# Kernel optimization log

Hardware: AMD Instinct MI355X
Metric: run time of the kernel (lower is better)

## Reference

```python
import jax, jax.numpy as jnp
import numpy as np

N_NODES = 100000
N_EDGES = 1600000
N_GRAPHS = 5000
NODE_DIM = 16
EDGE_DIM = 16
HID = 20


def setup_inputs() -> dict:
    key = jax.random.key(0)
    ks = jax.random.split(key, 12)
    edge_index = jax.random.randint(ks[0], (2, N_EDGES), 0, N_NODES)
    node_attr = jax.random.normal(ks[1], (N_NODES, NODE_DIM), dtype=jnp.float32)
    edge_attr = jax.random.normal(ks[2], (N_EDGES, EDGE_DIM), dtype=jnp.float32)
    batch = jnp.sort(jax.random.randint(ks[3], (N_NODES,), 0, N_GRAPHS))
    s = 0.1
    W_msg = jax.random.normal(ks[4], (2 * NODE_DIM + EDGE_DIM, HID), dtype=jnp.float32) * s
    b_msg = jnp.zeros((HID,), dtype=jnp.float32)
    W1 = jax.random.normal(ks[5], (HID, 10), dtype=jnp.float32) * s
    b1 = jnp.zeros((10,), dtype=jnp.float32)
    W2 = jax.random.normal(ks[6], (10, 10), dtype=jnp.float32) * s
    b2 = jnp.zeros((10,), dtype=jnp.float32)
    W3 = jax.random.normal(ks[7], (10, 1), dtype=jnp.float32) * s
    b3 = jnp.zeros((1,), dtype=jnp.float32)
    return {"edge_index": edge_index, "node_attr": node_attr, "edge_attr": edge_attr,
            "batch": batch, "W_msg": W_msg, "b_msg": b_msg, "W1": W1, "b1": b1,
            "W2": W2, "b2": b2, "W3": W3, "b3": b3}


def reference(edge_index, node_attr, edge_attr, batch,
              W_msg, b_msg, W1, b1, W2, b2, W3, b3):
    src, dst = edge_index[0], edge_index[1]
    # MPL_1: gather -> linear -> relu -> scatter-sum to destination nodes
    feats = jnp.concatenate([node_attr[src], node_attr[dst], edge_attr], axis=-1)  # [E, 48]
    msg = jax.nn.relu(feats @ W_msg + b_msg)  # [E, 20]
    x = jax.ops.segment_sum(msg, dst, num_segments=N_NODES)  # [N, 20]
    # node MLP + graph pooling (segment_coo sum over batch) + graph MLP
    x = jax.nn.relu(x @ W1 + b1)  # [N, 10]
    g = jax.ops.segment_sum(x, batch, num_segments=N_GRAPHS)  # [G, 10]
    g = jax.nn.relu(g @ W2 + b2)
    return g @ W3 + b3  # [G, 1]
```

## Files before the change

kernel.cpp:

```cpp
#include <hip/hip_runtime.h>

constexpr int NN = 100000;
constexpr int NE = 1600000;
constexpr int NG = 5000;
constexpr int BKT = 64;
constexpr int NBKT = (NN + BKT - 1) / BKT;
constexpr int NB = 128;
constexpr int CHUNK = NE / NB;

typedef float v2f __attribute__((ext_vector_type(2)));

constexpr size_t OFF_G  = 0;
constexpr size_t OFF_BH = 50048;
constexpr size_t OFF_ST = OFF_BH + (size_t)NB * NBKT;
constexpr size_t OFF_PM = OFF_ST + NBKT + 1;
constexpr size_t OFF_SP = OFF_PM + NE;
constexpr size_t OFF_EP = ((OFF_SP + NE) + 15) & ~(size_t)15;
constexpr size_t NEED_WORDS = OFF_EP + (size_t)NE * 16;

__global__ __launch_bounds__(256) void k_hist(const int* __restrict__ ei,
                                              int* __restrict__ bh,
                                              float* __restrict__ g) {
  __shared__ int lh[NBKT];
  for (int i = threadIdx.x; i < NBKT; i += 256) lh[i] = 0;
  __syncthreads();
  const int* dstp = ei + NE;
  int s = blockIdx.x * CHUNK;
  for (int i = s + threadIdx.x; i < s + CHUNK; i += 256)
    atomicAdd(&lh[dstp[i] >> 6], 1);
  int gid = blockIdx.x * 256 + threadIdx.x;
  if (gid < 12500) ((float4*)g)[gid] = make_float4(0.f, 0.f, 0.f, 0.f);
  __syncthreads();
  int* out = bh + (size_t)blockIdx.x * NBKT;
  for (int k = threadIdx.x; k < NBKT; k += 256) out[k] = lh[k];
}

__global__ __launch_bounds__(256) void k_btot(const int* __restrict__ bh,
                                              int* __restrict__ starts) {
  int k = blockIdx.x * 256 + threadIdx.x;
  if (k >= NBKT) return;
  int tot = 0;
  for (int b = 0; b < NB; b += 4) {
    int a0 = bh[(size_t)(b    ) * NBKT + k];
    int a1 = bh[(size_t)(b + 1) * NBKT + k];
    int a2 = bh[(size_t)(b + 2) * NBKT + k];
    int a3 = bh[(size_t)(b + 3) * NBKT + k];
    tot += a0 + a1 + a2 + a3;
  }
  starts[k] = tot;
}

__global__ __launch_bounds__(1024) void k_sscan(int* __restrict__ starts) {
  __shared__ int s0[1024], s1[1024];
  int t = threadIdx.x;
  int k0 = 2 * t, k1 = 2 * t + 1;
  int tot0 = (k0 < NBKT) ? starts[k0] : 0;
  int tot1 = (k1 < NBKT) ? starts[k1] : 0;
  int ssum = tot0 + tot1;
  int* cur = s0; int* nxt = s1;
  cur[t] = ssum;
  __syncthreads();
  for (int off = 1; off < 1024; off <<= 1) {
    int v = cur[t];
    if (t >= off) v += cur[t - off];
    nxt[t] = v;
    __syncthreads();
    int* tmp = cur; cur = nxt; nxt = tmp;
  }
  int excl = cur[t] - ssum;
  if (k0 < NBKT) starts[k0] = excl;
  if (k1 <= NBKT) starts[k1] = excl + tot0;
}

__global__ __launch_bounds__(256) void k_bases(int* __restrict__ bh,
                                               const int* __restrict__ starts) {
  int k = blockIdx.x * 256 + threadIdx.x;
  if (k >= NBKT) return;
  int run = starts[k];
  for (int b = 0; b < NB; ++b) {
    size_t idx = (size_t)b * NBKT + k;
    int v = bh[idx];
    bh[idx] = run;
    run += v;
  }
}

template <bool PRE>
__global__ __launch_bounds__(256) void k_scatter(const int* __restrict__ ei,
                                                 const int* __restrict__ bh,
                                                 int* __restrict__ pm) {
  __shared__ int base[NBKT];
  __shared__ int cnt[NBKT];
  const int* row = bh + (size_t)blockIdx.x * NBKT;
  for (int k = threadIdx.x; k < NBKT; k += 256) { base[k] = row[k]; cnt[k] = 0; }
  __syncthreads();
  const int* dstp = ei + NE;
  int s = blockIdx.x * CHUNK;
  for (int i = s + threadIdx.x; i < s + CHUNK; i += 256) {
    int d = dstp[i];
    int k = d >> 6;
    int r = atomicAdd(&cnt[k], 1);
    int slot = base[k] + r;
    if (PRE) pm[i] = slot | ((d & 63) << 25);
    else     pm[slot] = i | ((d & 63) << 24);
  }
}

__global__ __launch_bounds__(256) void k_reorder(const int* __restrict__ ei,
                                                 const float* __restrict__ eattr,
                                                 const int* __restrict__ inv,
                                                 float* __restrict__ ep_,
                                                 int* __restrict__ srcp) {
  int gid = blockIdx.x * 256 + threadIdx.x;
  int e = gid >> 2, part = gid & 3;
  if (e >= NE) return;
  int iv = inv[e];
  int slot = iv & 0x1FFFFFF;
  float4 v = ((const float4*)eattr)[(size_t)e * 4 + part];
  ((float4*)ep_)[(size_t)slot * 4 + part] = v;
  if (part == 0) srcp[slot] = ei[e] | ((iv >> 25) << 24);
}

#define PK4(V, K0) \
  a0 = __builtin_elementwise_fma(v2f{(V).x, (V).x}, W[K0+0], a0); \
  a1 = __builtin_elementwise_fma(v2f{(V).y, (V).y}, W[K0+1], a1); \
  a2 = __builtin_elementwise_fma(v2f{(V).z, (V).z}, W[K0+2], a2); \
  a3 = __builtin_elementwise_fma(v2f{(V).w, (V).w}, W[K0+3], a3);

template <bool PRE>
__global__ __launch_bounds__(256, 3) void k_edge(
    const int* __restrict__ ei,
    const float* __restrict__ nattr,
    const float* __restrict__ eattr,
    const float* __restrict__ Wm,
    const float* __restrict__ bm,
    const int* __restrict__ batch,
    const float* __restrict__ W1,
    const float* __restrict__ b1,
    const int* __restrict__ pm,
    const int* __restrict__ starts,
    float* __restrict__ g) {
  __shared__ float xt[20 * 65];
  __shared__ float gb[64 * 10];
  __shared__ float4 wt4[250];
  __shared__ float4 us4[64 * 5];
  __shared__ int s_se[2];
  __shared__ int s_bmin;
  int tid = threadIdx.x;
  for (int i = tid; i < 20 * 65; i += 256) xt[i] = 0.f;
  for (int i = tid; i < 640; i += 256) gb[i] = 0.f;
  if (tid < 240) {
    int j = tid / 24, t = tid - j * 24, k = 2 * t;
    wt4[j * 25 + t] = make_float4(Wm[k * 20 + 2 * j],       Wm[k * 20 + 2 * j + 1],
                                  Wm[(k + 1) * 20 + 2 * j], Wm[(k + 1) * 20 + 2 * j + 1]);
  }
  int nbase = blockIdx.x * BKT;
  {
    int dl = tid >> 2, part = tid & 3;
    int row = min(nbase + dl, NN - 1);
    us4[dl * 5 + part] = ((const float4*)nattr)[(size_t)row * 4 + part];
  }
  if (tid < 2) s_se[tid] = starts[blockIdx.x + tid];
  if (tid == 0) s_bmin = batch[nbase];
  __syncthreads();
  int is = s_se[0], ie = s_se[1];

  int wave = tid >> 6;
  int lane = tid & 63;
  int ep = lane / 10;
  int jp = lane - ep * 10;
  bool act = ep < 6;
  int epc = act ? ep : 0;

  v2f bj = {bm[2 * jp], bm[2 * jp + 1]};

  v2f W[48];
#pragma unroll
  for (int t = 0; t < 24; ++t) {
    float4 q = wt4[jp * 25 + t];
    W[2 * t]     = v2f{q.x, q.y};
    W[2 * t + 1] = v2f{q.z, q.w};
  }
#pragma unroll
  for (int k = 0; k < 48; ++k) asm volatile("" : "+v"(W[k]));

  int base = is + wave * 6;
  int sp0 = 0, sp1 = 0, sp2 = 0, sv0 = 0;
  if (base < ie) {
    sp0 = pm[min(base + epc, ie - 1)];
    sp1 = (base + 24 < ie) ? pm[min(base + 24 + epc, ie - 1)] : sp0;
    sp2 = (base + 48 < ie) ? pm[min(base + 48 + epc, ie - 1)] : sp1;
    if (!PRE) sv0 = ei[sp0 & 0xFFFFFF];
  }
  while (base < ie) {
    int sp3 = (base + 72 < ie) ? pm[min(base + 72 + epc, ie - 1)] : sp2;
    int svN = 0;
    if (!PRE) svN = (base + 24 < ie) ? ei[sp1 & 0xFFFFFF] : sv0;

    size_t eidx = PRE ? (size_t)min(base + epc, ie - 1)
                      : (size_t)(sp0 & 0xFFFFFF);
    int src = PRE ? (sp0 & 0xFFFFFF) : sv0;
    const float4* pe = (const float4*)eattr + eidx * 4;
    const float4* ps = (const float4*)nattr + (size_t)src * 4;
    float4 e0 = pe[0], e1 = pe[1], e2 = pe[2], e3 = pe[3];
    float4 n0 = ps[0], n1 = ps[1], n2 = ps[2], n3 = ps[3];
    int dl = (sp0 >> 24) & 63;
    float4 u0 = us4[dl * 5 + 0], u1 = us4[dl * 5 + 1];
    float4 u2 = us4[dl * 5 + 2], u3 = us4[dl * 5 + 3];

    v2f a0 = {0.f, 0.f}, a1 = {0.f, 0.f}, a2 = {0.f, 0.f}, a3 = {0.f, 0.f};
    PK4(n0, 0)  PK4(n1, 4)  PK4(n2, 8)  PK4(n3, 12)
    PK4(u0, 16) PK4(u1, 20) PK4(u2, 24) PK4(u3, 28)
    PK4(e0, 32) PK4(e1, 36) PK4(e2, 40) PK4(e3, 44)
    v2f r = ((a0 + a1) + (a2 + a3)) + bj;

    bool valid = act && (base + epc < ie);
    float m0 = fmaxf(r.x, 0.f);
    float m1 = fmaxf(r.y, 0.f);
    if (valid && m0 > 0.f) atomicAdd(&xt[(2 * jp) * 65 + dl], m0);
    if (valid && m1 > 0.f) atomicAdd(&xt[(2 * jp + 1) * 65 + dl], m1);

    base += 24; sp0 = sp1; sp1 = sp2; sp2 = sp3; sv0 = svN;
  }
  __syncthreads();

  int nn = min(BKT, NN - nbase);
  int bmin = s_bmin;
  if (tid < 64 && tid < nn) {
    int node = tid;
    float xi[20];
#pragma unroll
    for (int j = 0; j < 20; ++j) xi[j] = xt[j * 65 + node];
    float acc[10];
#pragma unroll
    for (int j = 0; j < 10; ++j) acc[j] = b1[j];
#pragma unroll
    for (int k = 0; k < 20; ++k) {
      float fk = xi[k];
#pragma unroll
      for (int j = 0; j < 10; ++j) acc[j] = fmaf(fk, W1[k * 10 + j], acc[j]);
    }
    int bn = batch[nbase + node];
    int d = bn - bmin;
    if (d < 64) {
#pragma unroll
      for (int j = 0; j < 10; ++j) {
        float m = fmaxf(acc[j], 0.f);
        if (m > 0.f) atomicAdd(&gb[d * 10 + j], m);
      }
    } else {
#pragma unroll
      for (int j = 0; j < 10; ++j) {
        float m = fmaxf(acc[j], 0.f);
        if (m > 0.f) unsafeAtomicAdd(&g[(size_t)bn * 10 + j], m);
      }
    }
  }
  __syncthreads();
  int glim = min(640, NG * 10 - bmin * 10);
  float* gp = g + (size_t)bmin * 10;
  for (int idx = tid; idx < glim; idx += 256) {
    float v = gb[idx];
    if (v != 0.f) unsafeAtomicAdd(&gp[idx], v);
  }
}

__global__ __launch_bounds__(256) void k_graph(
    const float* __restrict__ g,
    const float* __restrict__ W2, const float* __restrict__ b2,
    const float* __restrict__ W3, const float* __restrict__ b3,
    float* __restrict__ out) {
  int i = blockIdx.x * 256 + threadIdx.x;
  if (i >= NG) return;
  float gi[10];
  const float2* pg = (const float2*)(g + (size_t)i * 10);
#pragma unroll
  for (int k = 0; k < 5; ++k) { float2 v = pg[k]; gi[2*k] = v.x; gi[2*k+1] = v.y; }
  float o = b3[0];
#pragma unroll
  for (int j = 0; j < 10; ++j) {
    float a = b2[j];
#pragma unroll
    for (int k = 0; k < 10; ++k) a = fmaf(gi[k], W2[k * 10 + j], a);
    o = fmaf(fmaxf(a, 0.f), W3[j], o);
  }
  out[i] = o;
}

extern "C" void kernel_launch(void* const* d_in, const int* in_sizes, int n_in,
                              void* d_out, int out_size, void* d_ws, size_t ws_size,
                              hipStream_t stream) {
  const int*   ei    = (const int*)  d_in[0];
  const float* nattr = (const float*)d_in[1];
  const float* eattr = (const float*)d_in[2];
  const int*   batch = (const int*)  d_in[3];
  const float* Wm    = (const float*)d_in[4];
  const float* bm    = (const float*)d_in[5];
  const float* W1    = (const float*)d_in[6];
  const float* b1    = (const float*)d_in[7];
  const float* W2    = (const float*)d_in[8];
  const float* b2    = (const float*)d_in[9];
  const float* W3    = (const float*)d_in[10];
  const float* b3    = (const float*)d_in[11];

  float* g      = (float*)d_ws + OFF_G;
  int*   bh     = (int*)d_ws + OFF_BH;
  int*   starts = (int*)d_ws + OFF_ST;
  int*   pm     = (int*)d_ws + OFF_PM;
  int*   srcp   = (int*)d_ws + OFF_SP;
  float* ep_    = (float*)d_ws + OFF_EP;

  bool pre = ws_size >= NEED_WORDS * 4;

  constexpr int SCAN_BLKS = (NBKT + 255) / 256;

  k_hist   <<<NB, 256, 0, stream>>>(ei, bh, g);
  k_btot   <<<SCAN_BLKS, 256, 0, stream>>>(bh, starts);
  k_sscan  <<<1, 1024, 0, stream>>>(starts);
  k_bases  <<<SCAN_BLKS, 256, 0, stream>>>(bh, starts);
  if (pre) {
    k_scatter<true><<<NB, 256, 0, stream>>>(ei, bh, pm);
    k_reorder<<<(NE * 4 + 255) / 256, 256, 0, stream>>>(ei, eattr, pm, ep_, srcp);
    k_edge<true><<<NBKT, 256, 0, stream>>>(ei, nattr, ep_, Wm, bm, batch, W1, b1,
                                           srcp, starts, g);
  } else {
    k_scatter<false><<<NB, 256, 0, stream>>>(ei, bh, pm);
    k_edge<false><<<NBKT, 256, 0, stream>>>(ei, nattr, eattr, Wm, bm, batch, W1, b1,
                                            pm, starts, g);
  }
  k_graph  <<<(NG + 255) / 256, 256, 0, stream>>>(g, W2, b2, W3, b3, (float*)d_out);
}
```

Baseline: 382.7 us.

## Fuse edge reorder into scatter and software-pipeline edge/node loads in k_edge

```diff
diff --git a/kernel.cpp b/kernel.cpp
--- a/kernel.cpp
+++ b/kernel.cpp
@@ -88,7 +88,10 @@
 template <bool PRE>
 __global__ __launch_bounds__(256) void k_scatter(const int* __restrict__ ei,
                                                  const int* __restrict__ bh,
-                                                 int* __restrict__ pm) {
+                                                 int* __restrict__ pm,
+                                                 const float* __restrict__ eattr,
+                                                 float* __restrict__ ep_,
+                                                 int* __restrict__ srcp) {
   __shared__ int base[NBKT];
   __shared__ int cnt[NBKT];
   const int* row = bh + (size_t)blockIdx.x * NBKT;
@@ -101,24 +104,16 @@
     int k = d >> 6;
     int r = atomicAdd(&cnt[k], 1);
     int slot = base[k] + r;
-    if (PRE) pm[i] = slot | ((d & 63) << 25);
-    else     pm[slot] = i | ((d & 63) << 24);
-  }
-}
-
-__global__ __launch_bounds__(256) void k_reorder(const int* __restrict__ ei,
-                                                 const float* __restrict__ eattr,
-                                                 const int* __restrict__ inv,
-                                                 float* __restrict__ ep_,
-                                                 int* __restrict__ srcp) {
-  int gid = blockIdx.x * 256 + threadIdx.x;
-  int e = gid >> 2, part = gid & 3;
-  if (e >= NE) return;
-  int iv = inv[e];
-  int slot = iv & 0x1FFFFFF;
-  float4 v = ((const float4*)eattr)[(size_t)e * 4 + part];
-  ((float4*)ep_)[(size_t)slot * 4 + part] = v;
-  if (part == 0) srcp[slot] = ei[e] | ((iv >> 25) << 24);
+    if (PRE) {
+      srcp[slot] = ei[i] | ((d & 63) << 24);
+      const float4* src4 = (const float4*)eattr + (size_t)i * 4;
+      float4 v0 = src4[0], v1 = src4[1], v2 = src4[2], v3 = src4[3];
+      float4* dst4 = (float4*)ep_ + (size_t)slot * 4;
+      dst4[0] = v0; dst4[1] = v1; dst4[2] = v2; dst4[3] = v3;
+    } else {
+      pm[slot] = i | ((d & 63) << 24);
+    }
+  }
 }
 
 #define PK4(V, K0) \
@@ -128,7 +123,7 @@
   a3 = __builtin_elementwise_fma(v2f{(V).w, (V).w}, W[K0+3], a3);
 
 template <bool PRE>
-__global__ __launch_bounds__(256, 3) void k_edge(
+__global__ __launch_bounds__(256, 2) void k_edge(
     const int* __restrict__ ei,
     const float* __restrict__ nattr,
     const float* __restrict__ eattr,
@@ -185,42 +180,79 @@
   for (int k = 0; k < 48; ++k) asm volatile("" : "+v"(W[k]));
 
   int base = is + wave * 6;
-  int sp0 = 0, sp1 = 0, sp2 = 0, sv0 = 0;
-  if (base < ie) {
-    sp0 = pm[min(base + epc, ie - 1)];
-    sp1 = (base + 24 < ie) ? pm[min(base + 24 + epc, ie - 1)] : sp0;
-    sp2 = (base + 48 < ie) ? pm[min(base + 48 + epc, ie - 1)] : sp1;
-    if (!PRE) sv0 = ei[sp0 & 0xFFFFFF];
-  }
-  while (base < ie) {
-    int sp3 = (base + 72 < ie) ? pm[min(base + 72 + epc, ie - 1)] : sp2;
-    int svN = 0;
-    if (!PRE) svN = (base + 24 < ie) ? ei[sp1 & 0xFFFFFF] : sv0;
-
-    size_t eidx = PRE ? (size_t)min(base + epc, ie - 1)
-                      : (size_t)(sp0 & 0xFFFFFF);
-    int src = PRE ? (sp0 & 0xFFFFFF) : sv0;
-    const float4* pe = (const float4*)eattr + eidx * 4;
-    const float4* ps = (const float4*)nattr + (size_t)src * 4;
-    float4 e0 = pe[0], e1 = pe[1], e2 = pe[2], e3 = pe[3];
-    float4 n0 = ps[0], n1 = ps[1], n2 = ps[2], n3 = ps[3];
-    int dl = (sp0 >> 24) & 63;
-    float4 u0 = us4[dl * 5 + 0], u1 = us4[dl * 5 + 1];
-    float4 u2 = us4[dl * 5 + 2], u3 = us4[dl * 5 + 3];
-
-    v2f a0 = {0.f, 0.f}, a1 = {0.f, 0.f}, a2 = {0.f, 0.f}, a3 = {0.f, 0.f};
-    PK4(n0, 0)  PK4(n1, 4)  PK4(n2, 8)  PK4(n3, 12)
-    PK4(u0, 16) PK4(u1, 20) PK4(u2, 24) PK4(u3, 28)
-    PK4(e0, 32) PK4(e1, 36) PK4(e2, 40) PK4(e3, 44)
-    v2f r = ((a0 + a1) + (a2 + a3)) + bj;
-
-    bool valid = act && (base + epc < ie);
-    float m0 = fmaxf(r.x, 0.f);
-    float m1 = fmaxf(r.y, 0.f);
-    if (valid && m0 > 0.f) atomicAdd(&xt[(2 * jp) * 65 + dl], m0);
-    if (valid && m1 > 0.f) atomicAdd(&xt[(2 * jp + 1) * 65 + dl], m1);
-
-    base += 24; sp0 = sp1; sp1 = sp2; sp2 = sp3; sv0 = svN;
+  if (PRE) {
+    int sp0 = 0, sp1 = 0, sp2 = 0;
+    float4 e0, e1, e2, e3, n0, n1, n2, n3;
+    if (base < ie) {
+      sp0 = pm[min(base + epc, ie - 1)];
+      sp1 = (base + 24 < ie) ? pm[min(base + 24 + epc, ie - 1)] : sp0;
+      sp2 = (base + 48 < ie) ? pm[min(base + 48 + epc, ie - 1)] : sp1;
+      const float4* pe = (const float4*)eattr + (size_t)min(base + epc, ie - 1) * 4;
+      const float4* ps = (const float4*)nattr + (size_t)(sp0 & 0xFFFFFF) * 4;
+      e0 = pe[0]; e1 = pe[1]; e2 = pe[2]; e3 = pe[3];
+      n0 = ps[0]; n1 = ps[1]; n2 = ps[2]; n3 = ps[3];
+    }
+    while (base < ie) {
+      int sp3 = (base + 72 < ie) ? pm[min(base + 72 + epc, ie - 1)] : sp2;
+      const float4* peN = (const float4*)eattr + (size_t)min(base + 24 + epc, ie - 1) * 4;
+      const float4* psN = (const float4*)nattr + (size_t)(sp1 & 0xFFFFFF) * 4;
+      float4 e0N = peN[0], e1N = peN[1], e2N = peN[2], e3N = peN[3];
+      float4 n0N = psN[0], n1N = psN[1], n2N = psN[2], n3N = psN[3];
+
+      int dl = (sp0 >> 24) & 63;
+      float4 u0 = us4[dl * 5 + 0], u1 = us4[dl * 5 + 1];
+      float4 u2 = us4[dl * 5 + 2], u3 = us4[dl * 5 + 3];
+
+      v2f a0 = {0.f, 0.f}, a1 = {0.f, 0.f}, a2 = {0.f, 0.f}, a3 = {0.f, 0.f};
+      PK4(n0, 0)  PK4(n1, 4)  PK4(n2, 8)  PK4(n3, 12)
+      PK4(u0, 16) PK4(u1, 20) PK4(u2, 24) PK4(u3, 28)
+      PK4(e0, 32) PK4(e1, 36) PK4(e2, 40) PK4(e3, 44)
+      v2f r = ((a0 + a1) + (a2 + a3)) + bj;
+
+      bool valid = act && (base + epc < ie);
+      float m0 = fmaxf(r.x, 0.f);
+      float m1 = fmaxf(r.y, 0.f);
+      if (valid && m0 > 0.f) atomicAdd(&xt[(2 * jp) * 65 + dl], m0);
+      if (valid && m1 > 0.f) atomicAdd(&xt[(2 * jp + 1) * 65 + dl], m1);
+
+      base += 24; sp0 = sp1; sp1 = sp2; sp2 = sp3;
+      e0 = e0N; e1 = e1N; e2 = e2N; e3 = e3N;
+      n0 = n0N; n1 = n1N; n2 = n2N; n3 = n3N;
+    }
+  } else {
+    int sp0 = 0, sp1 = 0, sp2 = 0, sv0 = 0;
+    if (base < ie) {
+      sp0 = pm[min(base + epc, ie - 1)];
+      sp1 = (base + 24 < ie) ? pm[min(base + 24 + epc, ie - 1)] : sp0;
+      sp2 = (base + 48 < ie) ? pm[min(base + 48 + epc, ie - 1)] : sp1;
+      sv0 = ei[sp0 & 0xFFFFFF];
+    }
+    while (base < ie) {
+      int sp3 = (base + 72 < ie) ? pm[min(base + 72 + epc, ie - 1)] : sp2;
+      int svN = (base + 24 < ie) ? ei[sp1 & 0xFFFFFF] : sv0;
+
+      const float4* pe = (const float4*)eattr + (size_t)(sp0 & 0xFFFFFF) * 4;
+      const float4* ps = (const float4*)nattr + (size_t)sv0 * 4;
+      float4 e0 = pe[0], e1 = pe[1], e2 = pe[2], e3 = pe[3];
+      float4 n0 = ps[0], n1 = ps[1], n2 = ps[2], n3 = ps[3];
+      int dl = (sp0 >> 24) & 63;
+      float4 u0 = us4[dl * 5 + 0], u1 = us4[dl * 5 + 1];
+      float4 u2 = us4[dl * 5 + 2], u3 = us4[dl * 5 + 3];
+
+      v2f a0 = {0.f, 0.f}, a1 = {0.f, 0.f}, a2 = {0.f, 0.f}, a3 = {0.f, 0.f};
+      PK4(n0, 0)  PK4(n1, 4)  PK4(n2, 8)  PK4(n3, 12)
+      PK4(u0, 16) PK4(u1, 20) PK4(u2, 24) PK4(u3, 28)
+      PK4(e0, 32) PK4(e1, 36) PK4(e2, 40) PK4(e3, 44)
+      v2f r = ((a0 + a1) + (a2 + a3)) + bj;
+
+      bool valid = act && (base + epc < ie);
+      float m0 = fmaxf(r.x, 0.f);
+      float m1 = fmaxf(r.y, 0.f);
+      if (valid && m0 > 0.f) atomicAdd(&xt[(2 * jp) * 65 + dl], m0);
+      if (valid && m1 > 0.f) atomicAdd(&xt[(2 * jp + 1) * 65 + dl], m1);
+
+      base += 24; sp0 = sp1; sp1 = sp2; sp2 = sp3; sv0 = svN;
+    }
   }
   __syncthreads();
 
@@ -319,12 +351,11 @@
   k_sscan  <<<1, 1024, 0, stream>>>(starts);
   k_bases  <<<SCAN_BLKS, 256, 0, stream>>>(bh, starts);
   if (pre) {
-    k_scatter<true><<<NB, 256, 0, stream>>>(ei, bh, pm);
-    k_reorder<<<(NE * 4 + 255) / 256, 256, 0, stream>>>(ei, eattr, pm, ep_, srcp);
+    k_scatter<true><<<NB, 256, 0, stream>>>(ei, bh, pm, eattr, ep_, srcp);
     k_edge<true><<<NBKT, 256, 0, stream>>>(ei, nattr, ep_, Wm, bm, batch, W1, b1,
                                            srcp, starts, g);
   } else {
-    k_scatter<false><<<NB, 256, 0, stream>>>(ei, bh, pm);
+    k_scatter<false><<<NB, 256, 0, stream>>>(ei, bh, pm, eattr, ep_, srcp);
     k_edge<false><<<NBKT, 256, 0, stream>>>(ei, nattr, eattr, Wm, bm, batch, W1, b1,
                                             pm, starts, g);
   }
```

Measured after the change: 506.3 us. 32.3% more time.
